# Optimization experiments

Hardware: AMD Instinct MI355X
Metric: run time of the kernel (lower is better)

Reference implementation:

```python
import jax, jax.numpy as jnp
import numpy as np

B, N_IN, NV, F = 1, 65536, 1, 64
N_OUT, K = 16384, 16
N_DIST, N_PHI, OUT = 4, 8, 256
DIST_MAX = 0.1  # grid_layers[level_out].min_dist stand-in


def setup_inputs() -> dict:
    key = jax.random.key(0)
    ks = jax.random.split(key, 6)
    x = jax.random.normal(ks[0], (B, N_IN, NV, F), dtype=jnp.float32)
    nh_idx = jax.random.randint(ks[1], (N_OUT, K), 0, N_IN)  # neighbor gather indices
    d_dists = jax.random.uniform(ks[2], (N_OUT, K), dtype=jnp.float32) * DIST_MAX
    d_phi = jax.random.uniform(ks[3], (N_OUT, K), dtype=jnp.float32) * (2 * np.pi) - np.pi
    dists = jnp.linspace(0.0, DIST_MAX, N_DIST, dtype=jnp.float32)          # anchor distances
    sigma = jnp.asarray(DIST_MAX / 2, dtype=jnp.float32)                     # n_sigma == 1 -> scalar
    phi = jnp.linspace(-np.pi, np.pi, N_PHI + 1, dtype=jnp.float32)[:-1]     # von Mises: phi_min = -pi
    kappa = jnp.asarray(1.0, dtype=jnp.float32)                              # kappa_init
    W_out = jax.random.normal(ks[4], (F * N_DIST * N_PHI, OUT), dtype=jnp.float32) / np.sqrt(F * N_DIST * N_PHI)
    return {"x": x, "d_dists": d_dists, "d_phi": d_phi, "dists": dists,
            "sigma": sigma, "kappa": kappa, "phi": phi, "W_out": W_out, "nh_idx": nh_idx}


def reference(x, d_dists, d_phi, dists, sigma, kappa, phi, W_out, nh_idx):
    # Gaussian distance kernel: exp(-0.5*((d - dist_k)/sigma)^2)  -> (N_OUT, K, N_DIST)
    w_d = jnp.exp(-0.5 * ((d_dists[..., None] - dists) / sigma) ** 2)
    # von Mises angular kernel: exp(kappa * cos(d_phi - phi_p))   -> (N_OUT, K, N_PHI)
    w_p = jnp.exp(kappa * jnp.cos(d_phi[..., None] - phi))
    # combined kernel weights, normalized over the K neighbors per anchor
    w = w_d[..., :, None] * w_p[..., None, :]                      # (N_OUT, K, N_DIST, N_PHI)
    w = w / (jnp.sum(w, axis=1, keepdims=True) + 1e-9)
    w = w.reshape(N_OUT, K, N_DIST * N_PHI)                        # (N_OUT, K, M)
    # gather neighbor features from the input grid
    x_nb = x[:, nh_idx]                                            # (B, N_OUT, K, NV, F)
    # weighted aggregation over neighbors -> enhanced channels
    agg = jnp.einsum('bnkvf,nkm->bnvmf', x_nb, w)                  # (B, N_OUT, NV, M, F)
    agg = agg.reshape(B, N_OUT, NV, N_DIST * N_PHI * F)            # model_dim_enhanced = 2048
    return agg @ W_out                                             # (B, N_OUT, NV, OUT)
```

## Files before the change

### kernel.cpp

```cpp
#include <hip/hip_runtime.h>
#include <hip/hip_bf16.h>

#define N_IN   65536
#define N_OUTP 16384
#define KNB    16
#define FDIM   64
#define M_DIM  32
#define KDIM   2048
#define OUT_D  256

typedef __bf16 bf16x8_t __attribute__((ext_vector_type(8)));
typedef float  f32x4_t  __attribute__((ext_vector_type(4)));
typedef float  f32x2_t  __attribute__((ext_vector_type(2)));


__device__ __forceinline__ unsigned pk2(float a, float b) {
  __bf16 b0 = (__bf16)a, b1 = (__bf16)b;
  return ((unsigned)__builtin_bit_cast(unsigned short, b1) << 16) |
          (unsigned)__builtin_bit_cast(unsigned short, b0);
}

__global__ __launch_bounds__(256) void pack_B_kernel(
    const float* __restrict__ W, uint4* __restrict__ Bws)
{
  __shared__ float wlds[32 * 260];
  const int kk = blockIdx.x;
  const int t  = threadIdx.x;

  const float4* Wb = (const float4*)(W + kk * 32 * OUT_D);
#pragma unroll
  for (int i = 0; i < 8; ++i) {
    int idx = i * 256 + t;
    int row = idx >> 6, c4 = idx & 63;
    float4 v = Wb[idx];
    *(float4*)(wlds + row * 260 + c4 * 4) = v;
  }
  __syncthreads();

#pragma unroll
  for (int j = 0; j < 4; ++j) {
    int c  = j * 256 + t;
    int l  = c & 63, nt = c >> 6;
    int r0 = (l >> 4) * 8, col = nt * 16 + (l & 15);
    union { unsigned short s[8]; uint4 v; } u;
#pragma unroll
    for (int jj = 0; jj < 8; ++jj) {
      __bf16 b = (__bf16)wlds[(r0 + jj) * 260 + col];
      u.s[jj] = __builtin_bit_cast(unsigned short, b);
    }
    Bws[(size_t)kk * 1024 + c] = u.v;
  }
}

#define WST 580
#define WKS 36
#define XST 1092
#define XKS 68

__global__ __launch_bounds__(256) void agg_kernel(
    const float* __restrict__ x,
    const float* __restrict__ d_dists,
    const float* __restrict__ d_phi,
    const float* __restrict__ dists,
    const float* __restrict__ sigma_p,
    const float* __restrict__ kappa_p,
    const float* __restrict__ phi,
    const int*   __restrict__ nh_idx,
    uint4*       __restrict__ Aws)
{
  __shared__ __align__(16) float wbuf[8 * WST];
  __shared__ __align__(16) float xbuf[8 * XST];

  const int t  = threadIdx.x;
  const int n0 = blockIdx.x * 8;
  const int T  = blockIdx.x >> 1;
  const int r0 = (blockIdx.x & 1) * 8;

  const int h = t & 1, gk = (t >> 1) & 15, gr8 = t >> 5;
  const int gidx = nh_idx[(n0 + gr8) * KNB + gk];
  const float4* xr = (const float4*)x + (size_t)gidx * 16 + h * 8;
  float4 xreg[8];
#pragma unroll
  for (int j = 0; j < 8; ++j) xreg[j] = xr[j];

  {
    const float sinv = 1.0f / sigma_p[0];
    const float kap  = kappa_p[0];
    float phiv[8], distv[4];
#pragma unroll
    for (int p = 0; p < 8; ++p) phiv[p] = phi[p];
#pragma unroll
    for (int d = 0; d < 4; ++d) distv[d] = dists[d];

    int rk = t >> 1, r8 = rk >> 4, k = rk & 15, rep = t & 1;
    int n = n0 + r8;
    float dd = d_dists[n * KNB + k];
    float dp = d_phi[n * KNB + k];
    float wp[8];
#pragma unroll
    for (int p = 0; p < 8; ++p) wp[p] = __expf(kap * __cosf(dp - phiv[p]));
#pragma unroll
    for (int dl = 0; dl < 2; ++dl) {
      int d = rep * 2 + dl;
      float td = (dd - distv[d]) * sinv;
      float wd = __expf(-0.5f * td * td);
      float* dst = wbuf + r8 * WST + k * WKS + d * 8;
      *(float4*)(dst)     = make_float4(wd * wp[0], wd * wp[1], wd * wp[2], wd * wp[3]);
      *(float4*)(dst + 4) = make_float4(wd * wp[4], wd * wp[5], wd * wp[6], wd * wp[7]);
    }
  }

  {
    float4* xd = (float4*)(xbuf + gr8 * XST + gk * XKS + h * 36);
#pragma unroll
    for (int j = 0; j < 8; ++j) xd[j] = xreg[j];
  }
  __syncthreads();

  {
    int r8 = t >> 5, m = t & 31;
    float wv[16];
    float s = 0.f;
#pragma unroll
    for (int k = 0; k < 16; ++k) {
      wv[k] = wbuf[r8 * WST + k * WKS + m];
      s += wv[k];
    }
    float wn = 1.0f / (s + 1e-9f);
#pragma unroll
    for (int k = 0; k < 16; ++k)
      wbuf[r8 * WST + k * WKS + m] = wv[k] * wn;
  }
  __syncthreads();

  {
    const int r8 = t & 7, fo = (t >> 3) & 7, mq = t >> 6;
    f32x2_t acc[8][4];
#pragma unroll
    for (int mi = 0; mi < 8; ++mi)
#pragma unroll
      for (int fj = 0; fj < 4; ++fj) acc[mi][fj] = (f32x2_t){0.f, 0.f};

    const float* wp_ = wbuf + r8 * WST + mq * 8;
    const float* xp_ = xbuf + r8 * XST + ((fo < 4) ? fo * 8 : 36 + (fo - 4) * 8);

#pragma unroll 8
    for (int k = 0; k < 16; ++k) {
      float4 wa = *(const float4*)(wp_ + k * WKS);
      float4 wb = *(const float4*)(wp_ + k * WKS + 4);
      float4 xa = *(const float4*)(xp_ + k * XKS);
      float4 xb = *(const float4*)(xp_ + k * XKS + 4);
      float wv[8] = {wa.x, wa.y, wa.z, wa.w, wb.x, wb.y, wb.z, wb.w};
      f32x2_t xv[4] = {(f32x2_t){xa.x, xa.y}, (f32x2_t){xa.z, xa.w},
                       (f32x2_t){xb.x, xb.y}, (f32x2_t){xb.z, xb.w}};
#pragma unroll
      for (int mi = 0; mi < 8; ++mi) {
        f32x2_t wm = (f32x2_t){wv[mi], wv[mi]};
#pragma unroll
        for (int fj = 0; fj < 4; ++fj)
          acc[mi][fj] += wm * xv[fj];
      }
    }

    uint4* base = Aws + (size_t)T * 4096 + (fo & 3) * 16 + r0 + r8
                      + (size_t)(fo >> 2) * 64;
#pragma unroll
    for (int mi = 0; mi < 8; ++mi) {
      int m = mq * 8 + mi;
      uint4 v;
      v.x = pk2(acc[mi][0][0], acc[mi][0][1]);
      v.y = pk2(acc[mi][1][0], acc[mi][1][1]);
      v.z = pk2(acc[mi][2][0], acc[mi][2][1]);
      v.w = pk2(acc[mi][3][0], acc[mi][3][1]);
      base[m * 128] = v;
    }
  }
}

__global__ __launch_bounds__(256) void gemm_kernel(
    const uint4* __restrict__ Astream,
    const uint4* __restrict__ Bws,
    float*       __restrict__ out)
{
  const int t    = threadIdx.x;
  const int lane = t & 63;
  const int w    = t >> 6;
  const int rb   = blockIdx.x;

  const uint4* pa = Astream + (size_t)(rb * 4) * 4096 + lane;
  const uint4* pb = Bws + (w * 4) * 64 + lane;

  f32x4_t cacc[4][4];
#pragma unroll
  for (int mt = 0; mt < 4; ++mt)
#pragma unroll
    for (int i = 0; i < 4; ++i)
      cacc[mt][i] = (f32x4_t){0.f, 0.f, 0.f, 0.f};

  uint4 a[2][4], b[2][4];
#pragma unroll
  for (int s = 0; s < 2; ++s) {
#pragma unroll
    for (int mt = 0; mt < 4; ++mt) a[s][mt] = pa[mt * 4096 + s * 64];
#pragma unroll
    for (int i = 0; i < 4; ++i)    b[s][i]  = pb[s * 1024 + i * 64];
  }

#pragma unroll 4
  for (int kk = 0; kk < 64; ++kk) {
    const int s = kk & 1;
    bf16x8_t B0 = __builtin_bit_cast(bf16x8_t, b[s][0]);
    bf16x8_t B1 = __builtin_bit_cast(bf16x8_t, b[s][1]);
    bf16x8_t B2 = __builtin_bit_cast(bf16x8_t, b[s][2]);
    bf16x8_t B3 = __builtin_bit_cast(bf16x8_t, b[s][3]);
#pragma unroll
    for (int mt = 0; mt < 4; ++mt) {
      bf16x8_t A = __builtin_bit_cast(bf16x8_t, a[s][mt]);
      cacc[mt][0] = __builtin_amdgcn_mfma_f32_16x16x32_bf16(A, B0, cacc[mt][0], 0, 0, 0);
      cacc[mt][1] = __builtin_amdgcn_mfma_f32_16x16x32_bf16(A, B1, cacc[mt][1], 0, 0, 0);
      cacc[mt][2] = __builtin_amdgcn_mfma_f32_16x16x32_bf16(A, B2, cacc[mt][2], 0, 0, 0);
      cacc[mt][3] = __builtin_amdgcn_mfma_f32_16x16x32_bf16(A, B3, cacc[mt][3], 0, 0, 0);
    }
    if (kk < 62) {
#pragma unroll
      for (int mt = 0; mt < 4; ++mt) a[s][mt] = pa[mt * 4096 + (kk + 2) * 64];
#pragma unroll
      for (int i = 0; i < 4; ++i)    b[s][i]  = pb[(kk + 2) * 1024 + i * 64];
    }
  }

  const int rbase = rb * 64 + (lane >> 4) * 4;
  const int cbase = w * 64 + (lane & 15);
#pragma unroll
  for (int mt = 0; mt < 4; ++mt)
#pragma unroll
    for (int i = 0; i < 4; ++i)
#pragma unroll
      for (int reg = 0; reg < 4; ++reg)
        out[(rbase + mt * 16 + reg) * OUT_D + cbase + i * 16] = cacc[mt][i][reg];
}

extern "C" void kernel_launch(void* const* d_in, const int* in_sizes, int n_in,
                              void* d_out, int out_size, void* d_ws, size_t ws_size,
                              hipStream_t stream) {
  const float* x      = (const float*)d_in[0];
  const float* dd     = (const float*)d_in[1];
  const float* dp     = (const float*)d_in[2];
  const float* dists  = (const float*)d_in[3];
  const float* sigma  = (const float*)d_in[4];
  const float* kappa  = (const float*)d_in[5];
  const float* phi    = (const float*)d_in[6];
  const float* W      = (const float*)d_in[7];
  const int*   nh     = (const int*)d_in[8];
  float*       out    = (float*)d_out;

  uint4* Bws = (uint4*)d_ws;
  uint4* Aws = (uint4*)((char*)d_ws + (1 << 20));

  pack_B_kernel<<<64, 256, 0, stream>>>(W, Bws);
  agg_kernel<<<N_OUTP / 8, 256, 0, stream>>>(
      x, dd, dp, dists, sigma, kappa, phi, nh, Aws);
  gemm_kernel<<<N_OUTP / 64, 256, 0, stream>>>(Aws, Bws, out);
}
```

Measured before the change: 62.75 us.

## Split GEMM K dimension across two wave groups with LDS reduction

The GEMM block grows from 256 to 512 threads. The two halves of the waves each handle alternate K-steps, and their partial tiles are summed through shared memory before the output is written. The register prefetch depth rises from 2 to 4 stages. The aim is more waves in flight per block to hide global-load latency in a grid of only 256 blocks, at the cost of a 68 KB LDS reduction buffer and an extra barrier.

```diff
diff --git a/kernel.cpp b/kernel.cpp
--- a/kernel.cpp
+++ b/kernel.cpp
@@ -177,18 +177,22 @@
   }
 }
 
-__global__ __launch_bounds__(256) void gemm_kernel(
+__global__ __launch_bounds__(512, 2) void gemm_kernel(
     const uint4* __restrict__ Astream,
     const uint4* __restrict__ Bws,
     float*       __restrict__ out)
 {
+  __shared__ float red[4][64 * 68];
+
   const int t    = threadIdx.x;
   const int lane = t & 63;
   const int w    = t >> 6;
+  const int cg   = w & 3;
+  const int half = w >> 2;
   const int rb   = blockIdx.x;
 
-  const uint4* pa = Astream + (size_t)(rb * 4) * 4096 + lane;
-  const uint4* pb = Bws + (w * 4) * 64 + lane;
+  const uint4* pa = Astream + (size_t)(rb * 4) * 4096 + half * 64 + lane;
+  const uint4* pb = Bws + (half * 16 + cg * 4) * 64 + lane;
 
   f32x4_t cacc[4][4];
 #pragma unroll
@@ -197,18 +201,18 @@
     for (int i = 0; i < 4; ++i)
       cacc[mt][i] = (f32x4_t){0.f, 0.f, 0.f, 0.f};
 
-  uint4 a[2][4], b[2][4];
-#pragma unroll
-  for (int s = 0; s < 2; ++s) {
-#pragma unroll
-    for (int mt = 0; mt < 4; ++mt) a[s][mt] = pa[mt * 4096 + s * 64];
-#pragma unroll
-    for (int i = 0; i < 4; ++i)    b[s][i]  = pb[s * 1024 + i * 64];
+  uint4 a[4][4], b[4][4];
+#pragma unroll
+  for (int s = 0; s < 4; ++s) {
+#pragma unroll
+    for (int mt = 0; mt < 4; ++mt) a[s][mt] = pa[mt * 4096 + s * 128];
+#pragma unroll
+    for (int i = 0; i < 4; ++i)    b[s][i]  = pb[s * 2048 + i * 64];
   }
 
 #pragma unroll 4
-  for (int kk = 0; kk < 64; ++kk) {
-    const int s = kk & 1;
+  for (int j = 0; j < 32; ++j) {
+    const int s = j & 3;
     bf16x8_t B0 = __builtin_bit_cast(bf16x8_t, b[s][0]);
     bf16x8_t B1 = __builtin_bit_cast(bf16x8_t, b[s][1]);
     bf16x8_t B2 = __builtin_bit_cast(bf16x8_t, b[s][2]);
@@ -221,23 +225,40 @@
       cacc[mt][2] = __builtin_amdgcn_mfma_f32_16x16x32_bf16(A, B2, cacc[mt][2], 0, 0, 0);
       cacc[mt][3] = __builtin_amdgcn_mfma_f32_16x16x32_bf16(A, B3, cacc[mt][3], 0, 0, 0);
     }
-    if (kk < 62) {
-#pragma unroll
-      for (int mt = 0; mt < 4; ++mt) a[s][mt] = pa[mt * 4096 + (kk + 2) * 64];
-#pragma unroll
-      for (int i = 0; i < 4; ++i)    b[s][i]  = pb[(kk + 2) * 1024 + i * 64];
-    }
-  }
-
-  const int rbase = rb * 64 + (lane >> 4) * 4;
-  const int cbase = w * 64 + (lane & 15);
-#pragma unroll
-  for (int mt = 0; mt < 4; ++mt)
-#pragma unroll
-    for (int i = 0; i < 4; ++i)
-#pragma unroll
-      for (int reg = 0; reg < 4; ++reg)
-        out[(rbase + mt * 16 + reg) * OUT_D + cbase + i * 16] = cacc[mt][i][reg];
+    if (j < 28) {
+#pragma unroll
+      for (int mt = 0; mt < 4; ++mt) a[s][mt] = pa[mt * 4096 + (j + 4) * 128];
+#pragma unroll
+      for (int i = 0; i < 4; ++i)    b[s][i]  = pb[(j + 4) * 2048 + i * 64];
+    }
+  }
+
+  const int lrow = (lane >> 4) * 4;
+  const int lcol = lane & 15;
+
+  if (half == 0) {
+#pragma unroll
+    for (int mt = 0; mt < 4; ++mt)
+#pragma unroll
+      for (int i = 0; i < 4; ++i)
+#pragma unroll
+        for (int reg = 0; reg < 4; ++reg)
+          red[cg][(mt * 16 + lrow + reg) * 68 + i * 16 + lcol] = cacc[mt][i][reg];
+  }
+  __syncthreads();
+  if (half == 1) {
+#pragma unroll
+    for (int mt = 0; mt < 4; ++mt)
+#pragma unroll
+      for (int i = 0; i < 4; ++i)
+#pragma unroll
+        for (int reg = 0; reg < 4; ++reg) {
+          int row = mt * 16 + lrow + reg;
+          int col = i * 16 + lcol;
+          float v = red[cg][row * 68 + col] + cacc[mt][i][reg];
+          out[(rb * 64 + row) * OUT_D + cg * 64 + col] = v;
+        }
+  }
 }
 
 extern "C" void kernel_launch(void* const* d_in, const int* in_sizes, int n_in,
@@ -260,5 +281,5 @@
   pack_B_kernel<<<64, 256, 0, stream>>>(W, Bws);
   agg_kernel<<<N_OUTP / 8, 256, 0, stream>>>(
       x, dd, dp, dists, sigma, kappa, phi, nh, Aws);
-  gemm_kernel<<<N_OUTP / 64, 256, 0, stream>>>(Aws, Bws, out);
-}
+  gemm_kernel<<<N_OUTP / 64, 512, 0, stream>>>(Aws, Bws, out);
+}
```

After: 60.62 us. 1.04x faster.
